# Optimization experiments

Measured on AMD Instinct MI355X. Metric: run time of the kernel, lower is better.

## Reference

```python
import jax, jax.numpy as jnp
import numpy as np

M = 64            # multiplicity of 0e and 1o node irreps
NODE_DIM = M + 3 * M  # 256
NUM_BASIS = 8
CUTOFF = 5.0
HIDDEN = 64
NUM_W = 4 * M     # tp weight_numel: 4 uvu paths, M weights each
EPS = 1e-5


def setup_inputs() -> dict:
    key = jax.random.key(0)
    ks = jax.random.split(key, 16)
    N, E = 40000, 640000
    node_feats = jax.random.normal(ks[0], (N, NODE_DIM), dtype=jnp.float32)
    edge_index = jax.random.randint(ks[1], (2, E), 0, N)
    edge_vectors = jax.random.normal(ks[2], (E, 3), dtype=jnp.float32)
    edge_lengths = jax.random.uniform(ks[3], (E,), minval=0.5, maxval=CUTOFF, dtype=jnp.float32)
    # radial MLP params (num_basis -> hidden -> hidden -> NUM_W, SiLU)
    mlp_w1 = jax.random.normal(ks[4], (NUM_BASIS, HIDDEN), dtype=jnp.float32) / np.sqrt(NUM_BASIS)
    mlp_b1 = jnp.zeros((HIDDEN,), jnp.float32)
    mlp_w2 = jax.random.normal(ks[5], (HIDDEN, HIDDEN), dtype=jnp.float32) / np.sqrt(HIDDEN)
    mlp_b2 = jnp.zeros((HIDDEN,), jnp.float32)
    mlp_w3 = jax.random.normal(ks[6], (HIDDEN, NUM_W), dtype=jnp.float32) / np.sqrt(HIDDEN)
    mlp_b3 = jnp.zeros((NUM_W,), jnp.float32)
    # equivariant linear: per-irrep channel mixing
    lin_w0 = jax.random.normal(ks[7], (M, M), dtype=jnp.float32)
    lin_w1 = jax.random.normal(ks[8], (M, M), dtype=jnp.float32)
    # equivariant layer norm affine params
    gamma0 = jnp.ones((M,), jnp.float32)
    beta0 = jnp.zeros((M,), jnp.float32)
    gamma1 = jnp.ones((M,), jnp.float32)
    return dict(node_feats=node_feats, edge_index=edge_index, edge_vectors=edge_vectors,
                edge_lengths=edge_lengths, mlp_w1=mlp_w1, mlp_b1=mlp_b1, mlp_w2=mlp_w2,
                mlp_b2=mlp_b2, mlp_w3=mlp_w3, mlp_b3=mlp_b3, lin_w0=lin_w0, lin_w1=lin_w1,
                gamma0=gamma0, beta0=beta0, gamma1=gamma1)


def reference(node_feats, edge_index, edge_vectors, edge_lengths,
              mlp_w1, mlp_b1, mlp_w2, mlp_b2, mlp_w3, mlp_b3,
              lin_w0, lin_w1, gamma0, beta0, gamma1):
    N = node_feats.shape[0]
    row, col = edge_index[0], edge_index[1]

    # spherical harmonics of normalized edge vectors, 'component' normalization
    unit = edge_vectors / jnp.linalg.norm(edge_vectors, axis=-1, keepdims=True)
    sh1 = jnp.sqrt(3.0) * unit                                     # [E,3]; sh0 == 1

    # Bessel radial basis on edge lengths
    n = jnp.arange(1, NUM_BASIS + 1, dtype=node_feats.dtype)
    r = edge_lengths[:, None]
    rbf = jnp.sqrt(2.0 / CUTOFF) * jnp.sin(n * jnp.pi * r / CUTOFF) / r  # [E,B]

    # polynomial envelope (DimeNet, p=5)
    u = edge_lengths / CUTOFF
    env = jnp.where(u < 1.0, 1.0 - 21.0 * u**5 + 35.0 * u**6 - 15.0 * u**7, 0.0)[:, None]

    # radial MLP -> per-edge tensor-product weights, enveloped
    h = jax.nn.silu(rbf @ mlp_w1 + mlp_b1)
    h = jax.nn.silu(h @ mlp_w2 + mlp_b2)
    tp_w = (h @ mlp_w3 + mlp_b3) * env                             # [E, 4M]
    wa, wb, wc, wd = jnp.split(tp_w, 4, axis=-1)                   # each [E,M]

    # gather sender features
    s0 = node_feats[row, :M]                                       # [E,M]   0e block
    s1 = node_feats[row, M:].reshape(-1, M, 3)                     # [E,M,3] 1o block

    # weighted uvu tensor product, path-normalized (2 paths per output irrep)
    inv_s2 = 1.0 / jnp.sqrt(2.0)
    m0 = (wa * s0 + wd * jnp.einsum('emi,ei->em', s1, sh1)) * inv_s2        # [E,M]
    m1 = (wb[:, :, None] * s1 + wc[:, :, None] * s0[:, :, None] * sh1[:, None, :]) * inv_s2
    messages = jnp.concatenate([m0, m1.reshape(-1, 3 * M)], axis=-1)        # [E,256]

    # scatter-add to receivers
    agg = jax.ops.segment_sum(messages, col, num_segments=N)       # [N,256]

    # equivariant linear: mix multiplicities per irrep, fan-in normalized
    a0 = (agg[:, :M] @ lin_w0) / jnp.sqrt(jnp.asarray(M, node_feats.dtype))
    a1 = jnp.einsum('nmi,mk->nki', agg[:, M:].reshape(N, M, 3), lin_w1) \
         / jnp.sqrt(jnp.asarray(M, node_feats.dtype))

    # equivariant layer norm: standard LN on scalars, RMS-of-norms on vectors
    mu = a0.mean(axis=-1, keepdims=True)
    var = ((a0 - mu) ** 2).mean(axis=-1, keepdims=True)
    o0 = gamma0 * (a0 - mu) / jnp.sqrt(var + EPS) + beta0
    vnorm2 = (a1 ** 2).sum(-1)                                     # [N,M]
    rms = jnp.sqrt(vnorm2.mean(-1, keepdims=True) + EPS)           # [N,1]
    o1 = gamma1[None, :, None] * a1 / rms[:, :, None]

    out = jnp.concatenate([o0, o1.reshape(N, 3 * M)], axis=-1)
    return node_feats + out
```

## Files before the change

### kernel.cpp

```cpp
#include <hip/hip_runtime.h>
#include <hip/hip_fp16.h>

#define NDIM 256
#define LUT_N 4096
#define LUT_BLOCKS (LUT_N / 4)
#define SCAN_BLK 1024

typedef _Float16 h2 __attribute__((ext_vector_type(2)));
typedef __fp16   g2 __attribute__((ext_vector_type(2)));
union HU { unsigned u; h2 h; g2 g; };

__device__ __forceinline__ float fdot2f(unsigned a_bits, unsigned b_bits, float c)
{
    HU a, b; a.u = a_bits; b.u = b_bits;
#if __has_builtin(__builtin_amdgcn_fdot2)
    return __builtin_amdgcn_fdot2(a.h, b.h, c, false);
#else
    return fmaf((float)a.h.x, (float)b.h.x, fmaf((float)a.h.y, (float)b.h.y, c));
#endif
}

__global__ __launch_bounds__(256) void prep_kernel(
    const float* __restrict__ w1, const float* __restrict__ b1,
    const float* __restrict__ w2, const float* __restrict__ b2,
    const float* __restrict__ w3, const float* __restrict__ b3,
    uint2* __restrict__ lutp,
    const int* __restrict__ col, int E,
    int* __restrict__ counts, int* __restrict__ rank,
    const float* __restrict__ nf, uint2* __restrict__ nft,
    const float* __restrict__ lw0, const float* __restrict__ lw1,
    uint2* __restrict__ lwpk,
    int histBlocks, int tBlocks, int N)
{
    if (blockIdx.x >= (unsigned)(LUT_BLOCKS + histBlocks + tBlocks)) {
        int t = (blockIdx.x - LUT_BLOCKS - histBlocks - tBlocks) * 256 + threadIdx.x;
        if (t < 32 * 64) {
            int i = t >> 6, lane = t & 63;
            HU w0p, w1p;
            w0p.h = h2{(_Float16)lw0[(2 * i) * 64 + lane], (_Float16)lw0[(2 * i + 1) * 64 + lane]};
            w1p.h = h2{(_Float16)lw1[(2 * i) * 64 + lane], (_Float16)lw1[(2 * i + 1) * 64 + lane]};
            lwpk[t] = make_uint2(w0p.u, w1p.u);
        }
        return;
    }
    if (blockIdx.x >= (unsigned)(LUT_BLOCKS + histBlocks)) {
        int t = (blockIdx.x - LUT_BLOCKS - histBlocks) * 256 + threadIdx.x;
        if (t < N * 64) {
            int n = t >> 6, m = t & 63;
            const float* nr = nf + (size_t)n * NDIM;
            float s0 = nr[m];
            float3 s1 = ((const float3*)(nr + 64))[m];
            HU a, b;
            a.h = h2{(_Float16)s1.x, (_Float16)s1.y};
            b.h = h2{(_Float16)s1.z, (_Float16)s0};
            nft[t] = make_uint2(a.u, b.u);
        }
        return;
    }
    if (blockIdx.x >= (unsigned)LUT_BLOCKS) {
        int i = (blockIdx.x - LUT_BLOCKS) * 256 + threadIdx.x;
        if (i < E) rank[i] = atomicAdd(&counts[col[i]], 1);
        return;
    }

    __shared__ float h1s[4][64];
    __shared__ float h2s[4][64];
    int tid = threadIdx.x;
    int wave = tid >> 6;
    int j = tid & 63;
    int p = blockIdx.x * 4 + wave;
    float r = 0.5f + (4.5f / (float)(LUT_N - 1)) * (float)p;

    const float cnorm = 0.6324555320336759f;
    float acc = b1[j];
    #pragma unroll
    for (int k = 0; k < 8; ++k) {
        float freq = (float)(k + 1) * (3.14159265358979323846f / 5.0f);
        acc = fmaf(cnorm * sinf(freq * r) / r, w1[k * 64 + j], acc);
    }
    h1s[wave][j] = acc / (1.0f + expf(-acc));
    __syncthreads();

    acc = b2[j];
    #pragma unroll 8
    for (int m = 0; m < 64; ++m) acc = fmaf(h1s[wave][m], w2[m * 64 + j], acc);
    h2s[wave][j] = acc / (1.0f + expf(-acc));
    __syncthreads();

    float u = r * 0.2f;
    float u5 = u * u * u * u * u;
    float env = (u < 1.0f) ? (1.0f - 21.0f * u5 + 35.0f * u5 * u - 15.0f * u5 * u * u) : 0.0f;

    float o0 = b3[j], o1 = b3[64 + j], o2 = b3[128 + j], o3 = b3[192 + j];
    #pragma unroll 8
    for (int m = 0; m < 64; ++m) {
        float hv = h2s[wave][m];
        const float* wr = w3 + m * 256;
        o0 = fmaf(hv, wr[j],       o0);
        o1 = fmaf(hv, wr[64 + j],  o1);
        o2 = fmaf(hv, wr[128 + j], o2);
        o3 = fmaf(hv, wr[192 + j], o3);
    }
    HU uab, ucd;
    uab.h = h2{(_Float16)(o0 * env), (_Float16)(o1 * env)};
    ucd.h = h2{(_Float16)(o2 * env), (_Float16)(o3 * env)};
    lutp[p * 64 + j] = make_uint2(uab.u, ucd.u);
}

__global__ __launch_bounds__(SCAN_BLK) void scan1_kernel(
    const int* __restrict__ counts, int* __restrict__ loc,
    int* __restrict__ btot, int N)
{
    __shared__ int sh[SCAN_BLK];
    int t = threadIdx.x;
    int idx = blockIdx.x * SCAN_BLK + t;
    int v = (idx < N) ? counts[idx] : 0;
    sh[t] = v;
    __syncthreads();
    int acc = v;
    for (int o = 1; o < SCAN_BLK; o <<= 1) {
        int add = (t >= o) ? sh[t - o] : 0;
        __syncthreads();
        acc += add;
        sh[t] = acc;
        __syncthreads();
    }
    if (idx <= N) loc[idx] = acc - v;
    if (t == SCAN_BLK - 1) btot[blockIdx.x] = acc;
}

__device__ __forceinline__ int btot_scan(const int* __restrict__ btot, int nb, int lane)
{
    int v = (lane < nb) ? btot[lane] : 0;
    int acc = v;
    #pragma unroll
    for (int o = 1; o < 64; o <<= 1) {
        int up = __shfl_up(acc, o);
        if (lane >= o) acc += up;
    }
    return acc - v;
}

__global__ __launch_bounds__(256) void scatter_kernel(
    const int* __restrict__ row, const int* __restrict__ col,
    const float* __restrict__ evec, const float* __restrict__ elen,
    int E, const int* __restrict__ loc, const int* __restrict__ btot, int nb,
    const int* __restrict__ rank, uint4* __restrict__ em)
{
    int lane = threadIdx.x & 63;
    int excl = btot_scan(btot, nb, lane);

    int i = blockIdx.x * 256 + threadIdx.x;
    if (i < E) {
        int c = col[i];
        int p = loc[c] + __shfl(excl, c >> 10) + rank[i];
        float vx = evec[3 * i + 0], vy = evec[3 * i + 1], vz = evec[3 * i + 2];
        float inv = rsqrtf(vx * vx + vy * vy + vz * vz) * 1.7320508075688772f;
        float x = (elen[i] - 0.5f) * ((float)(LUT_N - 1) / 4.5f);
        int i0 = (int)(x + 0.5f);
        i0 = i0 < 0 ? 0 : (i0 > LUT_N - 1 ? LUT_N - 1 : i0);
        HU a, b;
        a.h = h2{(_Float16)(vx * inv), (_Float16)(vy * inv)};
        b.h = h2{(_Float16)(vz * inv), (_Float16)0.0f};
        unsigned packed = (unsigned)row[i] | ((unsigned)i0 << 16);
        em[p] = make_uint4(a.u, b.u, packed, 0u);
    }
}

struct St {
    uint2 L;
    uint2 sv;
    unsigned sh_xy, sh_z0;
};

__device__ __forceinline__ St stage_load(int j, int lane,
                                         const uint4* __restrict__ em,
                                         const uint2* __restrict__ lutp,
                                         const uint2* __restrict__ nft)
{
    St s;
    uint4 md = em[j];
    s.sh_xy = md.x;
    s.sh_z0 = md.y;
    int rsrc = (int)(md.z & 0xFFFFu);
    int i0 = (int)(md.z >> 16);
    s.L = lutp[i0 * 64 + lane];
    s.sv = nft[(size_t)rsrc * 64 + lane];
    return s;
}

__device__ __forceinline__ void accum_st(const St& s, float& acc0, float& accx,
                                         float& accy, float& accz)
{
    HU lab, lcd, svxy, svzs, shxy, shz0;
    lab.u = s.L.x;  lcd.u = s.L.y;
    svxy.u = s.sv.x; svzs.u = s.sv.y; shxy.u = s.sh_xy; shz0.u = s.sh_z0;

    float wa = (float)lab.h.x, wb = (float)lab.h.y;
    float wc = (float)lcd.h.x, wd = (float)lcd.h.y;

    float dot = fdot2f(s.sv.x, s.sh_xy, 0.0f);
    dot = fdot2f(s.sv.y, s.sh_z0, dot);

    float s0 = (float)svzs.h.y;
    acc0 = fmaf(wa, s0, fmaf(wd, dot, acc0));
    float wcs0 = wc * s0;
    accx = fmaf(wb, (float)svxy.h.x, fmaf(wcs0, (float)shxy.h.x, accx));
    accy = fmaf(wb, (float)svxy.h.y, fmaf(wcs0, (float)shxy.h.y, accy));
    accz = fmaf(wb, (float)svzs.h.x, fmaf(wcs0, (float)shz0.h.x, accz));
}

__global__ __launch_bounds__(256, 4) void node_kernel(
    const float* __restrict__ nf,
    const uint2* __restrict__ nft,
    const uint2* __restrict__ lutp,
    const int* __restrict__ loc,
    const int* __restrict__ btot, int nb,
    const uint4* __restrict__ em,
    const uint2* __restrict__ lwpk,
    const float* __restrict__ g0,
    const float* __restrict__ be0,
    const float* __restrict__ g1,
    float* __restrict__ out,
    int N)
{
    __shared__ uint4 agp[4][32];
    int tid = threadIdx.x;
    int wave = tid >> 6;
    int lane = tid & 63;
    int n = blockIdx.x * 4 + wave;

    int excl = btot_scan(btot, nb, lane);

    if (n >= N) return;

    int start = loc[n]     + __shfl(excl, n >> 10);
    int end   = loc[n + 1] + __shfl(excl, (n + 1) >> 10);
    start = __builtin_amdgcn_readfirstlane(start);
    end   = __builtin_amdgcn_readfirstlane(end);

    float acc0 = 0.0f, accx = 0.0f, accy = 0.0f, accz = 0.0f;

    int j = start;
    if (end - start >= 8) {
        St s0 = stage_load(j + 0, lane, em, lutp, nft);
        St s1 = stage_load(j + 1, lane, em, lutp, nft);
        St s2 = stage_load(j + 2, lane, em, lutp, nft);
        St s3 = stage_load(j + 3, lane, em, lutp, nft);
        St s4 = stage_load(j + 4, lane, em, lutp, nft);
        St s5 = stage_load(j + 5, lane, em, lutp, nft);
        St s6 = stage_load(j + 6, lane, em, lutp, nft);
        St s7 = stage_load(j + 7, lane, em, lutp, nft);
        j += 8;
        for (; j + 8 <= end; j += 8) {
            __builtin_amdgcn_sched_barrier(0);
            accum_st(s0, acc0, accx, accy, accz);
            accum_st(s1, acc0, accx, accy, accz);
            accum_st(s2, acc0, accx, accy, accz);
            accum_st(s3, acc0, accx, accy, accz);
            __builtin_amdgcn_sched_barrier(0);
            s0 = stage_load(j + 0, lane, em, lutp, nft);
            s1 = stage_load(j + 1, lane, em, lutp, nft);
            s2 = stage_load(j + 2, lane, em, lutp, nft);
            s3 = stage_load(j + 3, lane, em, lutp, nft);
            __builtin_amdgcn_sched_barrier(0);
            accum_st(s4, acc0, accx, accy, accz);
            accum_st(s5, acc0, accx, accy, accz);
            accum_st(s6, acc0, accx, accy, accz);
            accum_st(s7, acc0, accx, accy, accz);
            __builtin_amdgcn_sched_barrier(0);
            s4 = stage_load(j + 4, lane, em, lutp, nft);
            s5 = stage_load(j + 5, lane, em, lutp, nft);
            s6 = stage_load(j + 6, lane, em, lutp, nft);
            s7 = stage_load(j + 7, lane, em, lutp, nft);
        }
        __builtin_amdgcn_sched_barrier(0);
        accum_st(s0, acc0, accx, accy, accz);
        accum_st(s1, acc0, accx, accy, accz);
        accum_st(s2, acc0, accx, accy, accz);
        accum_st(s3, acc0, accx, accy, accz);
        accum_st(s4, acc0, accx, accy, accz);
        accum_st(s5, acc0, accx, accy, accz);
        accum_st(s6, acc0, accx, accy, accz);
        accum_st(s7, acc0, accx, accy, accz);
    }
    for (; j < end; ++j) {
        St s = stage_load(j, lane, em, lutp, nft);
        accum_st(s, acc0, accx, accy, accz);
    }

    const float INVS2 = 0.7071067811865476f;
    float v0 = acc0 * INVS2, v1 = accx * INVS2, v2 = accy * INVS2, v3 = accz * INVS2;
    float p0 = __shfl_xor(v0, 1);
    float p1 = __shfl_xor(v1, 1);
    float p2 = __shfl_xor(v2, 1);
    float p3 = __shfl_xor(v3, 1);
    if (!(lane & 1)) {
        HU u0, u1, u2, u3;
        u0.g = __builtin_amdgcn_cvt_pkrtz(v0, p0);
        u1.g = __builtin_amdgcn_cvt_pkrtz(v1, p1);
        u2.g = __builtin_amdgcn_cvt_pkrtz(v2, p2);
        u3.g = __builtin_amdgcn_cvt_pkrtz(v3, p3);
        agp[wave][lane >> 1] = make_uint4(u0.u, u1.u, u2.u, u3.u);
    }

    float a0 = 0.0f, t1x = 0.0f, t1y = 0.0f, t1z = 0.0f;
    #pragma unroll 8
    for (int i = 0; i < 32; ++i) {
        uint2 wp = lwpk[i * 64 + lane];
        uint4 gp = agp[wave][i];
        a0  = fdot2f(gp.x, wp.x, a0);
        t1x = fdot2f(gp.y, wp.y, t1x);
        t1y = fdot2f(gp.z, wp.y, t1y);
        t1z = fdot2f(gp.w, wp.y, t1z);
    }
    const float sc = 0.125f;
    a0 *= sc; t1x *= sc; t1y *= sc; t1z *= sc;

    float mu = a0;
    #pragma unroll
    for (int o = 32; o > 0; o >>= 1) mu += __shfl_xor(mu, o);
    mu *= (1.0f / 64.0f);
    float d = a0 - mu;
    float var = d * d;
    #pragma unroll
    for (int o = 32; o > 0; o >>= 1) var += __shfl_xor(var, o);
    var *= (1.0f / 64.0f);
    float o0 = g0[lane] * d * rsqrtf(var + 1e-5f) + be0[lane];

    float vn = t1x * t1x + t1y * t1y + t1z * t1z;
    float ms = vn;
    #pragma unroll
    for (int o = 32; o > 0; o >>= 1) ms += __shfl_xor(ms, o);
    ms *= (1.0f / 64.0f);
    float rinv = rsqrtf(ms + 1e-5f);
    float gg = g1[lane];

    size_t b = (size_t)n * NDIM;
    out[b + lane] = nf[b + lane] + o0;
    float3 rv = ((const float3*)(nf + b + 64))[lane];
    float3 ov;
    ov.x = rv.x + gg * t1x * rinv;
    ov.y = rv.y + gg * t1y * rinv;
    ov.z = rv.z + gg * t1z * rinv;
    ((float3*)(out + b + 64))[lane] = ov;
}

extern "C" void kernel_launch(void* const* d_in, const int* in_sizes, int n_in,
                              void* d_out, int out_size, void* d_ws, size_t ws_size,
                              hipStream_t stream)
{
    const float* nf   = (const float*)d_in[0];
    const int*   eidx = (const int*)d_in[1];
    const float* evec = (const float*)d_in[2];
    const float* elen = (const float*)d_in[3];
    const float* w1   = (const float*)d_in[4];
    const float* b1   = (const float*)d_in[5];
    const float* w2   = (const float*)d_in[6];
    const float* b2   = (const float*)d_in[7];
    const float* w3   = (const float*)d_in[8];
    const float* b3   = (const float*)d_in[9];
    const float* lw0  = (const float*)d_in[10];
    const float* lw1  = (const float*)d_in[11];
    const float* g0   = (const float*)d_in[12];
    const float* be0  = (const float*)d_in[13];
    const float* g1   = (const float*)d_in[14];

    int N = in_sizes[0] / NDIM;
    int E = in_sizes[3];

    int nb = (N + SCAN_BLK) / SCAN_BLK;

    char* ws = (char*)d_ws;
    size_t off_b = 0;
    auto align256 = [&]() { off_b = (off_b + 255) & ~(size_t)255; };
    uint2* lutp = (uint2*)(ws + off_b);   off_b += (size_t)LUT_N * 64 * 8;    align256();
    int* counts = (int*)(ws + off_b);     off_b += (size_t)N * 4;             align256();
    int* loc = (int*)(ws + off_b);        off_b += (size_t)(N + 1) * 4;       align256();
    int* btot = (int*)(ws + off_b);       off_b += (size_t)nb * 4;            align256();
    int* rank = (int*)(ws + off_b);       off_b += (size_t)E * 4;             align256();
    uint4* em = (uint4*)(ws + off_b);     off_b += (size_t)E * 16;            align256();
    uint2* nft = (uint2*)(ws + off_b);    off_b += (size_t)N * 64 * 8;        align256();
    uint2* lwpk = (uint2*)(ws + off_b);   off_b += (size_t)32 * 64 * 8;

    const int* row = eidx;
    const int* col = eidx + E;

    int histBlocks = (E + 255) / 256;
    int tBlocks = (N * 64 + 255) / 256;
    int lwBlocks = (32 * 64 + 255) / 256;

    hipMemsetAsync(counts, 0, (size_t)N * 4, stream);
    prep_kernel<<<LUT_BLOCKS + histBlocks + tBlocks + lwBlocks, 256, 0, stream>>>(
        w1, b1, w2, b2, w3, b3, lutp, col, E, counts, rank, nf, nft,
        lw0, lw1, lwpk, histBlocks, tBlocks, N);
    scan1_kernel<<<nb, SCAN_BLK, 0, stream>>>(counts, loc, btot, N);
    scatter_kernel<<<(E + 255) / 256, 256, 0, stream>>>(row, col, evec, elen, E,
                                                        loc, btot, nb, rank, em);
    node_kernel<<<(N + 3) / 4, 256, 0, stream>>>(nf, nft, lutp, loc, btot, nb, em,
                                                 lwpk, g0, be0, g1,
                                                 (float*)d_out, N);
}
```

Measured before the change: 149.4 us.

## Process nodes in descending-degree order to balance wave workloads

Builds a permutation of nodes sorted by in-degree (capped at 63, subbinned by low bits to spread atomics) using a counting sort. The counting sort uses atomic ranks in the scan kernel, a new single-block bin scan, and extra blocks in the scatter kernel. The node kernel then processes nodes through this order, so heavy nodes start first and waves in a block have similar edge counts, which reduces tail imbalance. It costs an extra kernel launch, atomics, and an indirection that breaks the sequential node locality of the output writes and node feature reads.

```diff
diff --git a/kernel.cpp b/kernel.cpp
--- a/kernel.cpp
+++ b/kernel.cpp
@@ -5,6 +5,7 @@
 #define LUT_N 4096
 #define LUT_BLOCKS (LUT_N / 4)
 #define SCAN_BLK 1024
+#define NBIN2 2048
 
 typedef _Float16 h2 __attribute__((ext_vector_type(2)));
 typedef __fp16   g2 __attribute__((ext_vector_type(2)));
@@ -109,12 +110,17 @@
 
 __global__ __launch_bounds__(SCAN_BLK) void scan1_kernel(
     const int* __restrict__ counts, int* __restrict__ loc,
-    int* __restrict__ btot, int N)
+    int* __restrict__ btot, int* __restrict__ nrank, int* __restrict__ dcnt, int N)
 {
     __shared__ int sh[SCAN_BLK];
     int t = threadIdx.x;
     int idx = blockIdx.x * SCAN_BLK + t;
     int v = (idx < N) ? counts[idx] : 0;
+    if (idx < N) {
+        int dcap = v > 63 ? 63 : v;
+        int b2 = ((63 - dcap) << 5) | (idx & 31);
+        nrank[idx] = atomicAdd(&dcnt[b2], 1);
+    }
     sh[t] = v;
     __syncthreads();
     int acc = v;
@@ -129,6 +135,28 @@
     if (t == SCAN_BLK - 1) btot[blockIdx.x] = acc;
 }
 
+__global__ __launch_bounds__(1024) void dscan_kernel(
+    const int* __restrict__ dcnt, int* __restrict__ dbase)
+{
+    __shared__ int sh[1024];
+    int t = threadIdx.x;
+    int v0 = dcnt[2 * t], v1 = dcnt[2 * t + 1];
+    int s = v0 + v1;
+    sh[t] = s;
+    __syncthreads();
+    int acc = s;
+    for (int o = 1; o < 1024; o <<= 1) {
+        int add = (t >= o) ? sh[t - o] : 0;
+        __syncthreads();
+        acc += add;
+        sh[t] = acc;
+        __syncthreads();
+    }
+    int excl = acc - s;
+    dbase[2 * t]     = excl;
+    dbase[2 * t + 1] = excl + v0;
+}
+
 __device__ __forceinline__ int btot_scan(const int* __restrict__ btot, int nb, int lane)
 {
     int v = (lane < nb) ? btot[lane] : 0;
@@ -145,8 +173,22 @@
     const int* __restrict__ row, const int* __restrict__ col,
     const float* __restrict__ evec, const float* __restrict__ elen,
     int E, const int* __restrict__ loc, const int* __restrict__ btot, int nb,
-    const int* __restrict__ rank, uint4* __restrict__ em)
-{
+    const int* __restrict__ rank, uint4* __restrict__ em,
+    const int* __restrict__ counts, const int* __restrict__ nrank,
+    const int* __restrict__ dbase, int* __restrict__ order,
+    int eBlocks, int N)
+{
+    if (blockIdx.x >= (unsigned)eBlocks) {
+        int t = (blockIdx.x - eBlocks) * 256 + threadIdx.x;
+        if (t < N) {
+            int deg = counts[t];
+            int dcap = deg > 63 ? 63 : deg;
+            int b2 = ((63 - dcap) << 5) | (t & 31);
+            order[dbase[b2] + nrank[t]] = t;
+        }
+        return;
+    }
+
     int lane = threadIdx.x & 63;
     int excl = btot_scan(btot, nb, lane);
 
@@ -218,6 +260,7 @@
     const int* __restrict__ btot, int nb,
     const uint4* __restrict__ em,
     const uint2* __restrict__ lwpk,
+    const int* __restrict__ order,
     const float* __restrict__ g0,
     const float* __restrict__ be0,
     const float* __restrict__ g1,
@@ -228,11 +271,12 @@
     int tid = threadIdx.x;
     int wave = tid >> 6;
     int lane = tid & 63;
-    int n = blockIdx.x * 4 + wave;
+    int slot = blockIdx.x * 4 + wave;
 
     int excl = btot_scan(btot, nb, lane);
 
-    if (n >= N) return;
+    if (slot >= N) return;
+    int n = order[slot];
 
     int start = loc[n]     + __shfl(excl, n >> 10);
     int end   = loc[n + 1] + __shfl(excl, (n + 1) >> 10);
@@ -375,10 +419,14 @@
     size_t off_b = 0;
     auto align256 = [&]() { off_b = (off_b + 255) & ~(size_t)255; };
     uint2* lutp = (uint2*)(ws + off_b);   off_b += (size_t)LUT_N * 64 * 8;    align256();
-    int* counts = (int*)(ws + off_b);     off_b += (size_t)N * 4;             align256();
+    int* counts = (int*)(ws + off_b);     off_b += (size_t)N * 4;
+    int* dcnt = (int*)(ws + off_b);       off_b += (size_t)NBIN2 * 4;         align256();
     int* loc = (int*)(ws + off_b);        off_b += (size_t)(N + 1) * 4;       align256();
     int* btot = (int*)(ws + off_b);       off_b += (size_t)nb * 4;            align256();
+    int* dbase = (int*)(ws + off_b);      off_b += (size_t)NBIN2 * 4;         align256();
     int* rank = (int*)(ws + off_b);       off_b += (size_t)E * 4;             align256();
+    int* nrank = (int*)(ws + off_b);      off_b += (size_t)N * 4;             align256();
+    int* order = (int*)(ws + off_b);      off_b += (size_t)N * 4;             align256();
     uint4* em = (uint4*)(ws + off_b);     off_b += (size_t)E * 16;            align256();
     uint2* nft = (uint2*)(ws + off_b);    off_b += (size_t)N * 64 * 8;        align256();
     uint2* lwpk = (uint2*)(ws + off_b);   off_b += (size_t)32 * 64 * 8;
@@ -389,15 +437,20 @@
     int histBlocks = (E + 255) / 256;
     int tBlocks = (N * 64 + 255) / 256;
     int lwBlocks = (32 * 64 + 255) / 256;
-
-    hipMemsetAsync(counts, 0, (size_t)N * 4, stream);
+    int eBlocks = (E + 255) / 256;
+    int nBlocks = (N + 255) / 256;
+
+    hipMemsetAsync(counts, 0, ((size_t)N + NBIN2) * 4, stream);
     prep_kernel<<<LUT_BLOCKS + histBlocks + tBlocks + lwBlocks, 256, 0, stream>>>(
         w1, b1, w2, b2, w3, b3, lutp, col, E, counts, rank, nf, nft,
         lw0, lw1, lwpk, histBlocks, tBlocks, N);
-    scan1_kernel<<<nb, SCAN_BLK, 0, stream>>>(counts, loc, btot, N);
-    scatter_kernel<<<(E + 255) / 256, 256, 0, stream>>>(row, col, evec, elen, E,
-                                                        loc, btot, nb, rank, em);
+    scan1_kernel<<<nb, SCAN_BLK, 0, stream>>>(counts, loc, btot, nrank, dcnt, N);
+    dscan_kernel<<<1, 1024, 0, stream>>>(dcnt, dbase);
+    scatter_kernel<<<eBlocks + nBlocks, 256, 0, stream>>>(row, col, evec, elen, E,
+                                                          loc, btot, nb, rank, em,
+                                                          counts, nrank, dbase, order,
+                                                          eBlocks, N);
     node_kernel<<<(N + 3) / 4, 256, 0, stream>>>(nf, nft, lutp, loc, btot, nb, em,
-                                                 lwpk, g0, be0, g1,
+                                                 lwpk, order, g0, be0, g1,
                                                  (float*)d_out, N);
 }
```

Measured after the change: 169.3 us. 1.13x slower.
